# Kernel tuning notes

Measured on AMD Instinct MI355X. Metric: run time of the kernel, lower is better.

## Reference

```python
import jax, jax.numpy as jnp
import numpy as np

K = 10.0           # sigmoid sharpness (init arg k)
EPS = 1e-10


def setup_inputs() -> dict:
    key = jax.random.key(0)
    k1, k2 = jax.random.split(key)
    TOTAL = 8388608
    BATCH = 8192
    sub_logits = jax.random.normal(k1, (TOTAL, 3), dtype=jnp.float32)
    original_indices = jax.random.randint(k2, (TOTAL,), 0, BATCH, dtype=jnp.int64)
    return {"sub_logits": sub_logits, "original_indices": original_indices, "batch_size": BATCH}


def reference(sub_logits, original_indices, batch_size):
    # Note: the original computes softmax(sub_logits) into sub_probs but never
    # uses it; it does not affect the output, so it is omitted here.
    # Segment sums over sub-images belonging to each original image.
    s1 = jax.ops.segment_sum(sub_logits[:, 1] + sub_logits[:, 2],
                             original_indices, num_segments=batch_size)
    s0 = jax.ops.segment_sum(sub_logits[:, 0],
                             original_indices, num_segments=batch_size)
    logits_1 = jnp.log(jax.nn.sigmoid(K * (1.0 - s1)) + EPS)
    logits_0 = jnp.log(jax.nn.sigmoid(K * (5.0 - s0)) + EPS)
    return jnp.stack([logits_1, logits_0], axis=1)  # [batch_size, 2]
```

## Files before the change

### kernel.cpp

```cpp
#include <hip/hip_runtime.h>
#include <math.h>


constexpr float KSHARP   = 10.0f;
constexpr float EPS      = 1e-10f;
constexpr int   SEG      = 8192;
constexpr int   S2       = 2 * SEG;
constexpr float SCALE    = 2097152.0f;
constexpr float INV_SCALE = 1.0f / 2097152.0f;

__global__ __launch_bounds__(1024, 8) void seg_partial_kernel(
    const float* __restrict__ logits, const int* __restrict__ idx,
    int* __restrict__ partials, int n, int chunk)
{
    __shared__ int s1[SEG];
    __shared__ int s0[SEG];
    {
        int4 z = make_int4(0, 0, 0, 0);
        int4* p1 = (int4*)s1; int4* p0 = (int4*)s0;
        for (int i = threadIdx.x; i < SEG / 4; i += blockDim.x) { p1[i] = z; p0[i] = z; }
    }
    __syncthreads();

    long long cs = (long long)blockIdx.x * chunk;
    long long ce = cs + chunk; if (ce > n) ce = n;
    if (cs < ce) {
        int rows = (int)(ce - cs);
        int ngr  = rows >> 2;
        for (int g = threadIdx.x; g < ngr; g += blockDim.x) {
            long long r = cs + ((long long)g << 2);
            const float4* p = (const float4*)(logits + 3 * r);
            float4 a = p[0], b = p[1], c = p[2];
            int4 id = *(const int4*)(idx + r);
            atomicAdd(&s1[id.x], __float2int_rn((a.y + a.z) * SCALE));
            atomicAdd(&s0[id.x], __float2int_rn(a.x * SCALE));
            atomicAdd(&s1[id.y], __float2int_rn((b.x + b.y) * SCALE));
            atomicAdd(&s0[id.y], __float2int_rn(a.w * SCALE));
            atomicAdd(&s1[id.z], __float2int_rn((b.w + c.x) * SCALE));
            atomicAdd(&s0[id.z], __float2int_rn(b.z * SCALE));
            atomicAdd(&s1[id.w], __float2int_rn((c.z + c.w) * SCALE));
            atomicAdd(&s0[id.w], __float2int_rn(c.y * SCALE));
        }
        int tail = rows & 3;
        if ((int)threadIdx.x < tail) {
            long long r = cs + ((long long)ngr << 2) + threadIdx.x;
            float l0 = logits[3 * r], l1 = logits[3 * r + 1], l2 = logits[3 * r + 2];
            int b = idx[r];
            atomicAdd(&s1[b], __float2int_rn((l1 + l2) * SCALE));
            atomicAdd(&s0[b], __float2int_rn(l0 * SCALE));
        }
    }
    __syncthreads();
    int4* dst = (int4*)(partials + (size_t)blockIdx.x * S2);
    const int4* p1 = (const int4*)s1;
    const int4* p0 = (const int4*)s0;
    for (int i = threadIdx.x; i < SEG / 4; i += blockDim.x) dst[i] = p1[i];
    for (int i = threadIdx.x; i < SEG / 4; i += blockDim.x) dst[SEG / 4 + i] = p0[i];
}

__global__ __launch_bounds__(1024) void reduce_finalize_kernel(
    const int* __restrict__ partials, float* __restrict__ out,
    int nb, int batch)
{
    int col4 = blockIdx.x * 64 + threadIdx.x;
    const int4* p4 = (const int4*)partials;
    long long a0 = 0, a1 = 0, a2 = 0, a3 = 0;
    for (int b = threadIdx.y; b < nb; b += 16) {
        int4 v = p4[(size_t)b * (S2 / 4) + col4];
        a0 += v.x; a1 += v.y; a2 += v.z; a3 += v.w;
    }
    __shared__ long long red[16][64][4];
    red[threadIdx.y][threadIdx.x][0] = a0;
    red[threadIdx.y][threadIdx.x][1] = a1;
    red[threadIdx.y][threadIdx.x][2] = a2;
    red[threadIdx.y][threadIdx.x][3] = a3;
    __syncthreads();
    if (threadIdx.y == 0) {
        long long t0 = 0, t1 = 0, t2 = 0, t3 = 0;
        #pragma unroll
        for (int y = 0; y < 16; ++y) {
            t0 += red[y][threadIdx.x][0];
            t1 += red[y][threadIdx.x][1];
            t2 += red[y][threadIdx.x][2];
            t3 += red[y][threadIdx.x][3];
        }
        long long tot[4] = {t0, t1, t2, t3};
        #pragma unroll
        for (int q = 0; q < 4; ++q) {
            int j = col4 * 4 + q;
            float s = (float)tot[q] * INV_SCALE;
            bool is_s1 = (j < SEG);
            int  b     = is_s1 ? j : j - SEG;
            if (b < batch) {
                float C = is_s1 ? 1.0f : 5.0f;
                float x = KSHARP * (C - s);
                float sig;
                if (x >= 0.0f) { sig = 1.0f / (1.0f + expf(-x)); }
                else           { float e = expf(x); sig = e / (1.0f + e); }
                out[2 * b + (is_s1 ? 0 : 1)] = logf(sig + EPS);
            }
        }
    }
}

__global__ void accum_atomic_kernel(const float* __restrict__ logits,
                                    const int* __restrict__ idx,
                                    float* __restrict__ sums, int n)
{
    int tid = blockIdx.x * blockDim.x + threadIdx.x;
    int stride = gridDim.x * blockDim.x;
    for (long long r = tid; r < n; r += stride) {
        float l0 = logits[3 * r], l1 = logits[3 * r + 1], l2 = logits[3 * r + 2];
        int b = idx[r];
        atomicAdd(&sums[2 * b],     l1 + l2);
        atomicAdd(&sums[2 * b + 1], l0);
    }
}

__global__ void finalize_kernel(const float* __restrict__ sums,
                                float* __restrict__ out, int total)
{
    int j = blockIdx.x * blockDim.x + threadIdx.x;
    if (j >= total) return;
    float s = sums[j];
    float C = (j & 1) ? 5.0f : 1.0f;
    float x = KSHARP * (C - s);
    float sig;
    if (x >= 0.0f) { sig = 1.0f / (1.0f + expf(-x)); }
    else           { float e = expf(x); sig = e / (1.0f + e); }
    out[j] = logf(sig + EPS);
}

extern "C" void kernel_launch(void* const* d_in, const int* in_sizes, int n_in,
                              void* d_out, int out_size, void* d_ws, size_t ws_size,
                              hipStream_t stream) {
    const float* logits = (const float*)d_in[0];
    const int*   idx    = (const int*)d_in[1];
    int n     = in_sizes[1];
    int batch = out_size / 2;
    float* out = (float*)d_out;

    size_t bytes_per_block = (size_t)S2 * sizeof(int);
    int nb_max = (int)(ws_size / bytes_per_block);
    int nb = nb_max < 512 ? nb_max : 512;

    if (batch <= SEG && nb >= 8) {
        long long chunk_ll = ((long long)n + nb - 1) / nb;
        int chunk = (int)((chunk_ll + 3) & ~3LL);
        int* partials = (int*)d_ws;
        seg_partial_kernel<<<nb, 1024, 0, stream>>>(logits, idx, partials, n, chunk);

        dim3 rb(64, 16);
        reduce_finalize_kernel<<<S2 / 256, rb, 0, stream>>>(partials, out, nb, batch);
    } else {
        float* sums = (float*)d_ws;
        hipMemsetAsync(sums, 0, (size_t)2 * batch * sizeof(float), stream);
        int threads = 256;
        int blocks = (n + threads - 1) / threads;
        if (blocks > 2048) blocks = 2048;
        accum_atomic_kernel<<<blocks, threads, 0, stream>>>(logits, idx, sums, n);
        int total = 2 * batch;
        finalize_kernel<<<(total + 255) / 256, 256, 0, stream>>>(sums, out, total);
    }
}
```

Baseline: 43.76 us.

## Pack both segment sums and a row count into one 64-bit shared atomic

Each row's two fixed-point values are biased into 22-bit fields with a magic-number FMA and packed, together with a count bit, into one 64-bit word. This halves the number of shared-memory atomics per row. The reducer removes the bias using the per-block count. Precision drops from a 2^21 scale to a 2^17 scale, and field overflow is guarded by requiring chunk <= 4*batch, otherwise the old path is used.

```diff
diff --git a/kernel.cpp b/kernel.cpp
--- a/kernel.cpp
+++ b/kernel.cpp
@@ -2,12 +2,117 @@
 #include <math.h>
 
 
-constexpr float KSHARP   = 10.0f;
-constexpr float EPS      = 1e-10f;
-constexpr int   SEG      = 8192;
-constexpr int   S2       = 2 * SEG;
-constexpr float SCALE    = 2097152.0f;
-constexpr float INV_SCALE = 1.0f / 2097152.0f;
+constexpr float KSHARP = 10.0f;
+constexpr float EPS    = 1e-10f;
+constexpr int   SEG    = 8192;
+constexpr int   S2     = 2 * SEG;
+
+constexpr float SCALE     = 131072.0f;
+constexpr float INV_SCALE = 1.0f / 131072.0f;
+constexpr float MAGIC     = 2097152.0f + 8388608.0f;
+constexpr long long BIAS_I = 2097152;
+
+__device__ __forceinline__ unsigned fix22(float v) {
+    float f = __builtin_fmaf(v, SCALE, MAGIC);
+    return __float_as_uint(f) & 0x3FFFFFu;
+}
+
+__device__ __forceinline__ unsigned long long pack_row(float v1, float v0) {
+    return ((unsigned long long)fix22(v1) << 37)
+         | ((unsigned long long)fix22(v0) << 10) | 1ull;
+}
+
+__global__ __launch_bounds__(1024, 8) void seg_pack_kernel(
+    const float* __restrict__ logits, const int* __restrict__ idx,
+    unsigned long long* __restrict__ partials, int n, int chunk)
+{
+    __shared__ unsigned long long acc[SEG];
+    for (int i = threadIdx.x; i < SEG; i += blockDim.x) acc[i] = 0ull;
+    __syncthreads();
+
+    int cs = blockIdx.x * chunk;
+    int ce = cs + chunk; if (ce > n) ce = n;
+    if (cs < ce) {
+        int rows = ce - cs;
+        int ngr  = rows >> 2;
+        for (int g = threadIdx.x; g < ngr; g += blockDim.x) {
+            int r = cs + (g << 2);
+            const float4* p = (const float4*)(logits + 3 * (size_t)r);
+            float4 a = p[0], b = p[1], c = p[2];
+            int4 id = *(const int4*)(idx + r);
+            atomicAdd(&acc[id.x], pack_row(a.y + a.z, a.x));
+            atomicAdd(&acc[id.y], pack_row(b.x + b.y, a.w));
+            atomicAdd(&acc[id.z], pack_row(b.w + c.x, b.z));
+            atomicAdd(&acc[id.w], pack_row(c.z + c.w, c.y));
+        }
+        int tail = rows & 3;
+        if ((int)threadIdx.x < tail) {
+            int r = cs + (ngr << 2) + threadIdx.x;
+            float l0 = logits[3 * (size_t)r], l1 = logits[3 * (size_t)r + 1],
+                  l2 = logits[3 * (size_t)r + 2];
+            atomicAdd(&acc[idx[r]], pack_row(l1 + l2, l0));
+        }
+    }
+    __syncthreads();
+    int4* dst = (int4*)(partials + (size_t)blockIdx.x * SEG);
+    const int4* src = (const int4*)acc;
+    for (int i = threadIdx.x; i < SEG / 2; i += blockDim.x) dst[i] = src[i];
+}
+
+__global__ __launch_bounds__(1024) void reduce_pack_kernel(
+    const unsigned long long* __restrict__ partials, float* __restrict__ out,
+    int nb, int batch)
+{
+    int col2 = blockIdx.x * 64 + threadIdx.x;
+    long long s1a = 0, s0a = 0, s1b = 0, s0b = 0;
+    for (int b = threadIdx.y; b < nb; b += 16) {
+        const unsigned long long* row = partials + (size_t)b * SEG + 2 * col2;
+        unsigned long long u0 = row[0];
+        unsigned long long u1 = row[1];
+        long long K0 = (long long)(u0 & 0x3FFull);
+        long long K1 = (long long)(u1 & 0x3FFull);
+        s0a += (long long)((u0 >> 10) & 0x7FFFFFFull) - K0 * BIAS_I;
+        s1a += (long long)(u0 >> 37)                  - K0 * BIAS_I;
+        s0b += (long long)((u1 >> 10) & 0x7FFFFFFull) - K1 * BIAS_I;
+        s1b += (long long)(u1 >> 37)                  - K1 * BIAS_I;
+    }
+    __shared__ long long red[16][64][4];
+    red[threadIdx.y][threadIdx.x][0] = s1a;
+    red[threadIdx.y][threadIdx.x][1] = s0a;
+    red[threadIdx.y][threadIdx.x][2] = s1b;
+    red[threadIdx.y][threadIdx.x][3] = s0b;
+    __syncthreads();
+    if (threadIdx.y == 0) {
+        long long t[4] = {0, 0, 0, 0};
+        #pragma unroll
+        for (int y = 0; y < 16; ++y) {
+            t[0] += red[y][threadIdx.x][0];
+            t[1] += red[y][threadIdx.x][1];
+            t[2] += red[y][threadIdx.x][2];
+            t[3] += red[y][threadIdx.x][3];
+        }
+        #pragma unroll
+        for (int q = 0; q < 2; ++q) {
+            int j = 2 * col2 + q;
+            if (j < batch) {
+                float s1 = (float)t[2 * q]     * INV_SCALE;
+                float s0 = (float)t[2 * q + 1] * INV_SCALE;
+                float x1 = KSHARP * (1.0f - s1);
+                float x0 = KSHARP * (5.0f - s0);
+                float sg1, sg0;
+                if (x1 >= 0.0f) { sg1 = 1.0f / (1.0f + expf(-x1)); }
+                else            { float e = expf(x1); sg1 = e / (1.0f + e); }
+                if (x0 >= 0.0f) { sg0 = 1.0f / (1.0f + expf(-x0)); }
+                else            { float e = expf(x0); sg0 = e / (1.0f + e); }
+                out[2 * j + 0] = logf(sg1 + EPS);
+                out[2 * j + 1] = logf(sg0 + EPS);
+            }
+        }
+    }
+}
+
+constexpr float SCALE21     = 2097152.0f;
+constexpr float INV_SCALE21 = 1.0f / 2097152.0f;
 
 __global__ __launch_bounds__(1024, 8) void seg_partial_kernel(
     const float* __restrict__ logits, const int* __restrict__ idx,
@@ -21,7 +126,6 @@
         for (int i = threadIdx.x; i < SEG / 4; i += blockDim.x) { p1[i] = z; p0[i] = z; }
     }
     __syncthreads();
-
     long long cs = (long long)blockIdx.x * chunk;
     long long ce = cs + chunk; if (ce > n) ce = n;
     if (cs < ce) {
@@ -32,22 +136,22 @@
             const float4* p = (const float4*)(logits + 3 * r);
             float4 a = p[0], b = p[1], c = p[2];
             int4 id = *(const int4*)(idx + r);
-            atomicAdd(&s1[id.x], __float2int_rn((a.y + a.z) * SCALE));
-            atomicAdd(&s0[id.x], __float2int_rn(a.x * SCALE));
-            atomicAdd(&s1[id.y], __float2int_rn((b.x + b.y) * SCALE));
-            atomicAdd(&s0[id.y], __float2int_rn(a.w * SCALE));
-            atomicAdd(&s1[id.z], __float2int_rn((b.w + c.x) * SCALE));
-            atomicAdd(&s0[id.z], __float2int_rn(b.z * SCALE));
-            atomicAdd(&s1[id.w], __float2int_rn((c.z + c.w) * SCALE));
-            atomicAdd(&s0[id.w], __float2int_rn(c.y * SCALE));
+            atomicAdd(&s1[id.x], __float2int_rn((a.y + a.z) * SCALE21));
+            atomicAdd(&s0[id.x], __float2int_rn(a.x * SCALE21));
+            atomicAdd(&s1[id.y], __float2int_rn((b.x + b.y) * SCALE21));
+            atomicAdd(&s0[id.y], __float2int_rn(a.w * SCALE21));
+            atomicAdd(&s1[id.z], __float2int_rn((b.w + c.x) * SCALE21));
+            atomicAdd(&s0[id.z], __float2int_rn(b.z * SCALE21));
+            atomicAdd(&s1[id.w], __float2int_rn((c.z + c.w) * SCALE21));
+            atomicAdd(&s0[id.w], __float2int_rn(c.y * SCALE21));
         }
         int tail = rows & 3;
         if ((int)threadIdx.x < tail) {
             long long r = cs + ((long long)ngr << 2) + threadIdx.x;
             float l0 = logits[3 * r], l1 = logits[3 * r + 1], l2 = logits[3 * r + 2];
             int b = idx[r];
-            atomicAdd(&s1[b], __float2int_rn((l1 + l2) * SCALE));
-            atomicAdd(&s0[b], __float2int_rn(l0 * SCALE));
+            atomicAdd(&s1[b], __float2int_rn((l1 + l2) * SCALE21));
+            atomicAdd(&s0[b], __float2int_rn(l0 * SCALE21));
         }
     }
     __syncthreads();
@@ -76,19 +180,18 @@
     red[threadIdx.y][threadIdx.x][3] = a3;
     __syncthreads();
     if (threadIdx.y == 0) {
-        long long t0 = 0, t1 = 0, t2 = 0, t3 = 0;
+        long long t[4] = {0, 0, 0, 0};
         #pragma unroll
         for (int y = 0; y < 16; ++y) {
-            t0 += red[y][threadIdx.x][0];
-            t1 += red[y][threadIdx.x][1];
-            t2 += red[y][threadIdx.x][2];
-            t3 += red[y][threadIdx.x][3];
-        }
-        long long tot[4] = {t0, t1, t2, t3};
+            t[0] += red[y][threadIdx.x][0];
+            t[1] += red[y][threadIdx.x][1];
+            t[2] += red[y][threadIdx.x][2];
+            t[3] += red[y][threadIdx.x][3];
+        }
         #pragma unroll
         for (int q = 0; q < 4; ++q) {
             int j = col4 * 4 + q;
-            float s = (float)tot[q] * INV_SCALE;
+            float s = (float)t[q] * INV_SCALE21;
             bool is_s1 = (j < SEG);
             int  b     = is_s1 ? j : j - SEG;
             if (b < batch) {
@@ -140,18 +243,24 @@
     int batch = out_size / 2;
     float* out = (float*)d_out;
 
-    size_t bytes_per_block = (size_t)S2 * sizeof(int);
-    int nb_max = (int)(ws_size / bytes_per_block);
+    size_t bpb_pack = (size_t)SEG * 8;
+    int nb_max = (int)(ws_size / bpb_pack);
     int nb = nb_max < 512 ? nb_max : 512;
 
     if (batch <= SEG && nb >= 8) {
         long long chunk_ll = ((long long)n + nb - 1) / nb;
         int chunk = (int)((chunk_ll + 3) & ~3LL);
-        int* partials = (int*)d_ws;
-        seg_partial_kernel<<<nb, 1024, 0, stream>>>(logits, idx, partials, n, chunk);
-
-        dim3 rb(64, 16);
-        reduce_finalize_kernel<<<S2 / 256, rb, 0, stream>>>(partials, out, nb, batch);
+        if (chunk <= 4 * batch) {
+            unsigned long long* partials = (unsigned long long*)d_ws;
+            seg_pack_kernel<<<nb, 1024, 0, stream>>>(logits, idx, partials, n, chunk);
+            dim3 rb(64, 16);
+            reduce_pack_kernel<<<SEG / 128, rb, 0, stream>>>(partials, out, nb, batch);
+        } else {
+            int* partials = (int*)d_ws;
+            seg_partial_kernel<<<nb, 1024, 0, stream>>>(logits, idx, partials, n, chunk);
+            dim3 rb(64, 16);
+            reduce_finalize_kernel<<<S2 / 256, rb, 0, stream>>>(partials, out, nb, batch);
+        }
     } else {
         float* sums = (float*)d_ws;
         hipMemsetAsync(sums, 0, (size_t)2 * batch * sizeof(float), stream);
```

After: 45.71 us. +4.5%, slower.
